# Performance work log

Measured on AMD Instinct MI355X. Metric: run time of the kernel, lower is better.

The kernel has to match this reference:

```python
import jax, jax.numpy as jnp
import numpy as np

MARGIN = 1.0  # init kwarg margin; top_k=None; reduction='mean'


def setup_inputs() -> dict:
    key = jax.random.key(0)
    k1, k2, k3 = jax.random.split(key, 3)
    B, H = 16384, 64
    scores = jax.random.normal(k1, (B, H), dtype=jnp.float32)
    rankings = jax.random.randint(k2, (B, H), 0, 65, dtype=jnp.int32)
    mask = jax.random.randint(k3, (B, H), 0, 2, dtype=jnp.int32).astype(jnp.bool_)
    return {"scores": scores, "rankings": rankings, "mask": mask}


def reference(scores, rankings, mask):
    # valid horses: present in race AND have a positive ranking
    valid = mask & (rankings > 0)                      # [B,H]
    # pair (i,j) counts iff both valid and rank_i < rank_j (implies i!=j)
    pair = (valid[:, :, None] & valid[:, None, :]
            & (rankings[:, :, None] < rankings[:, None, :]))  # [B,H,H]
    # hinge: clamp(margin - (s_i - s_j), min=0)
    hinge = jnp.maximum(MARGIN - (scores[:, :, None] - scores[:, None, :]), 0.0)
    pair_f = pair.astype(scores.dtype)
    num_pairs = pair_f.sum(axis=(1, 2))                # [B]
    batch_loss = (hinge * pair_f).sum(axis=(1, 2)) / jnp.maximum(num_pairs, 1.0)
    has = (num_pairs > 0).astype(scores.dtype)         # races contributing to mean
    n_valid = has.sum()
    total = (batch_loss * has).sum()
    # reduction='mean' over races with at least one pair; 0.0 if none
    return jnp.where(n_valid > 0, total / jnp.maximum(n_valid, 1.0),
                     jnp.asarray(0.0, scores.dtype))
```

## Files before the change

kernel.cpp:

```cpp
#include <hip/hip_runtime.h>

#define H 64
#define WPB 4
#define BLOCKS 1024

__global__ __launch_bounds__(WPB * 64)
void prl_races(const float* __restrict__ scores,
               const int* __restrict__ rankings,
               const int* __restrict__ mask,
               float2* __restrict__ partial, int B)
{
    __shared__ float4 smem[WPB][H / 2];
    __shared__ float wsum[WPB], wcnt[WPB];

    const int lane   = threadIdx.x & 63;
    const int wv     = threadIdx.x >> 6;
    const int gwave  = blockIdx.x * WPB + wv;
    const int nwaves = gridDim.x * WPB;
    const int iters  = (B + nwaves - 1) / nwaves;

    float loc_sum = 0.0f, loc_has = 0.0f;

    for (int it = 0; it < iters; ++it) {
        const int race  = gwave + it * nwaves;
        const bool act  = race < B;

        float s = 0.0f;
        int key = 0;
        if (act) {
            const int idx = race * H + lane;
            s = scores[idx];
            const int r = rankings[idx];
            const int m = mask[idx];
            key = (m != 0 && r > 0) ? r : 0;
        }

        float2* sm2 = reinterpret_cast<float2*>(&smem[wv][0]);
        sm2[lane] = make_float2(s, __int_as_float(key));
        __syncthreads();

        const float t = 1.0f - s;
        float sum = 0.0f, cnt = 0.0f;
        #pragma unroll
        for (int jj = 0; jj < H / 2; ++jj) {
            const float4 p = smem[wv][jj];
            const int k0 = __float_as_int(p.y);
            const int k1 = __float_as_int(p.w);
            const float h0 = fmaxf(t + p.x, 0.0f);
            const float h1 = fmaxf(t + p.z, 0.0f);
            if (key < k0) { sum += h0; cnt += 1.0f; }
            if (key < k1) { sum += h1; cnt += 1.0f; }
        }
        if (key == 0) { sum = 0.0f; cnt = 0.0f; }

        #pragma unroll
        for (int off = 32; off > 0; off >>= 1) {
            sum += __shfl_down(sum, off, 64);
            cnt += __shfl_down(cnt, off, 64);
        }
        if (lane == 0 && cnt > 0.0f) {
            loc_sum += sum / cnt;
            loc_has += 1.0f;
        }
        __syncthreads();
    }

    if (lane == 0) { wsum[wv] = loc_sum; wcnt[wv] = loc_has; }
    __syncthreads();
    if (threadIdx.x == 0) {
        float s = 0.0f, c = 0.0f;
        #pragma unroll
        for (int w = 0; w < WPB; ++w) { s += wsum[w]; c += wcnt[w]; }
        partial[blockIdx.x] = make_float2(s, c);
    }
}

__global__ __launch_bounds__(256)
void prl_reduce(const float2* __restrict__ partial, float* __restrict__ out, int n)
{
    __shared__ float ss[4], sc[4];
    const int lane = threadIdx.x & 63;
    const int wv   = threadIdx.x >> 6;

    float s = 0.0f, c = 0.0f;
    for (int i = threadIdx.x; i < n; i += 256) {
        const float2 p = partial[i];
        s += p.x; c += p.y;
    }
    #pragma unroll
    for (int off = 32; off > 0; off >>= 1) {
        s += __shfl_down(s, off, 64);
        c += __shfl_down(c, off, 64);
    }
    if (lane == 0) { ss[wv] = s; sc[wv] = c; }
    __syncthreads();
    if (threadIdx.x == 0) {
        float ts = ss[0] + ss[1] + ss[2] + ss[3];
        float tc = sc[0] + sc[1] + sc[2] + sc[3];
        out[0] = (tc > 0.0f) ? ts / tc : 0.0f;
    }
}

extern "C" void kernel_launch(void* const* d_in, const int* in_sizes, int n_in,
                              void* d_out, int out_size, void* d_ws, size_t ws_size,
                              hipStream_t stream)
{
    const float* scores   = (const float*)d_in[0];
    const int*   rankings = (const int*)d_in[1];
    const int*   mask     = (const int*)d_in[2];
    const int B = in_sizes[0] / H;

    float2* partial = (float2*)d_ws;

    prl_races<<<BLOCKS, WPB * 64, 0, stream>>>(scores, rankings, mask, partial, B);
    prl_reduce<<<1, 256, 0, stream>>>(partial, (float*)d_out, BLOCKS);
}
```

Before: 76.56 us.

## Use packed fp16 pairwise math with fdot2 and process two races per wave

Switches the pairwise hinge and rank-comparison computation to packed half-precision. Rank comparisons become clamped differences and are folded into an fdot2 accumulation. Each wave now loads two races up front into per-race shared buffers, the in-loop __syncthreads are dropped, and the grid grows to 2048 blocks. Converting scores and ranks to fp16 loses precision in the hinge and can break rank comparisons, since the clamped difference only works as a step function for integer ranks. The per-race count is accumulated in fp16 and the final partial reduce now reads more partials.

```diff
diff --git a/kernel.cpp b/kernel.cpp
--- a/kernel.cpp
+++ b/kernel.cpp
@@ -2,7 +2,12 @@
 
 #define H 64
 #define WPB 4
-#define BLOCKS 1024
+#define RPW 2
+
+typedef _Float16 h2 __attribute__((ext_vector_type(2)));
+typedef _Float16 __attribute__((may_alias)) f16a;
+
+union U32H2 { unsigned int u; h2 h; };
 
 __global__ __launch_bounds__(WPB * 64)
 void prl_races(const float* __restrict__ scores,
@@ -10,48 +15,68 @@
                const int* __restrict__ mask,
                float2* __restrict__ partial, int B)
 {
-    __shared__ float4 smem[WPB][H / 2];
+    __shared__ uint4 smem[WPB][RPW][H / 4];
     __shared__ float wsum[WPB], wcnt[WPB];
 
     const int lane   = threadIdx.x & 63;
     const int wv     = threadIdx.x >> 6;
     const int gwave  = blockIdx.x * WPB + wv;
     const int nwaves = gridDim.x * WPB;
-    const int iters  = (B + nwaves - 1) / nwaves;
+
+    float s[RPW]; int key[RPW];
+    #pragma unroll
+    for (int it = 0; it < RPW; ++it) {
+        const int race = gwave + it * nwaves;
+        s[it] = 0.0f; key[it] = 0;
+        if (race < B) {
+            const int idx = race * H + lane;
+            s[it] = scores[idx];
+            const int r = rankings[idx];
+            const int m = mask[idx];
+            key[it] = (m != 0 && r > 0) ? r : 0;
+        }
+        char* wbase = (char*)&smem[wv][it][0];
+        const int g = lane >> 2, sl = (lane & 3) * 2;
+        *(f16a*)(wbase + g * 16 + sl)     = (_Float16)s[it];
+        *(f16a*)(wbase + g * 16 + 8 + sl) = (_Float16)(float)key[it];
+    }
 
     float loc_sum = 0.0f, loc_has = 0.0f;
 
-    for (int it = 0; it < iters; ++it) {
-        const int race  = gwave + it * nwaves;
-        const bool act  = race < B;
+    #pragma unroll
+    for (int it = 0; it < RPW; ++it) {
+        const h2 t2   = (h2)(_Float16)(1.0f - s[it]);
+        const h2 ki2  = (h2)(_Float16)(float)key[it];
+        const h2 zero = (h2)(_Float16)0.0f;
+        const h2 one  = (h2)(_Float16)1.0f;
 
-        float s = 0.0f;
-        int key = 0;
-        if (act) {
-            const int idx = race * H + lane;
-            s = scores[idx];
-            const int r = rankings[idx];
-            const int m = mask[idx];
-            key = (m != 0 && r > 0) ? r : 0;
+        float sumA = 0.0f, sumB = 0.0f;
+        h2 cntA = zero, cntB = zero;
+
+        #pragma unroll
+        for (int g = 0; g < H / 4; ++g) {
+            const uint4 q = smem[wv][it][g];
+            U32H2 ux, uy, uz, uw;
+            ux.u = q.x; uy.u = q.y; uz.u = q.z; uw.u = q.w;
+            const h2 hA = __builtin_elementwise_max(t2 + ux.h, zero);
+            const h2 hB = __builtin_elementwise_max(t2 + uy.h, zero);
+            const h2 pA = __builtin_elementwise_min(__builtin_elementwise_max(uz.h - ki2, zero), one);
+            const h2 pB = __builtin_elementwise_min(__builtin_elementwise_max(uw.h - ki2, zero), one);
+#if __has_builtin(__builtin_amdgcn_fdot2)
+            sumA = __builtin_amdgcn_fdot2(hA, pA, sumA, false);
+            sumB = __builtin_amdgcn_fdot2(hB, pB, sumB, false);
+#else
+            sumA += (float)hA.x * (float)pA.x + (float)hA.y * (float)pA.y;
+            sumB += (float)hB.x * (float)pB.x + (float)hB.y * (float)pB.y;
+#endif
+            cntA = cntA + pA;
+            cntB = cntB + pB;
         }
 
-        float2* sm2 = reinterpret_cast<float2*>(&smem[wv][0]);
-        sm2[lane] = make_float2(s, __int_as_float(key));
-        __syncthreads();
-
-        const float t = 1.0f - s;
-        float sum = 0.0f, cnt = 0.0f;
-        #pragma unroll
-        for (int jj = 0; jj < H / 2; ++jj) {
-            const float4 p = smem[wv][jj];
-            const int k0 = __float_as_int(p.y);
-            const int k1 = __float_as_int(p.w);
-            const float h0 = fmaxf(t + p.x, 0.0f);
-            const float h1 = fmaxf(t + p.z, 0.0f);
-            if (key < k0) { sum += h0; cnt += 1.0f; }
-            if (key < k1) { sum += h1; cnt += 1.0f; }
-        }
-        if (key == 0) { sum = 0.0f; cnt = 0.0f; }
+        float sum = sumA + sumB;
+        const h2 c2 = cntA + cntB;
+        float cnt = (float)c2.x + (float)c2.y;
+        if (key[it] == 0) { sum = 0.0f; cnt = 0.0f; }
 
         #pragma unroll
         for (int off = 32; off > 0; off >>= 1) {
@@ -62,16 +87,15 @@
             loc_sum += sum / cnt;
             loc_has += 1.0f;
         }
-        __syncthreads();
     }
 
     if (lane == 0) { wsum[wv] = loc_sum; wcnt[wv] = loc_has; }
     __syncthreads();
     if (threadIdx.x == 0) {
-        float s = 0.0f, c = 0.0f;
+        float ps = 0.0f, pc = 0.0f;
         #pragma unroll
-        for (int w = 0; w < WPB; ++w) { s += wsum[w]; c += wcnt[w]; }
-        partial[blockIdx.x] = make_float2(s, c);
+        for (int w = 0; w < WPB; ++w) { ps += wsum[w]; pc += wcnt[w]; }
+        partial[blockIdx.x] = make_float2(ps, pc);
     }
 }
 
@@ -95,8 +119,8 @@
     if (lane == 0) { ss[wv] = s; sc[wv] = c; }
     __syncthreads();
     if (threadIdx.x == 0) {
-        float ts = ss[0] + ss[1] + ss[2] + ss[3];
-        float tc = sc[0] + sc[1] + sc[2] + sc[3];
+        const float ts = ss[0] + ss[1] + ss[2] + ss[3];
+        const float tc = sc[0] + sc[1] + sc[2] + sc[3];
         out[0] = (tc > 0.0f) ? ts / tc : 0.0f;
     }
 }
@@ -112,6 +136,7 @@
 
     float2* partial = (float2*)d_ws;
 
-    prl_races<<<BLOCKS, WPB * 64, 0, stream>>>(scores, rankings, mask, partial, B);
-    prl_reduce<<<1, 256, 0, stream>>>(partial, (float*)d_out, BLOCKS);
+    const int grid = (B + WPB * RPW - 1) / (WPB * RPW);
+    prl_races<<<grid, WPB * 64, 0, stream>>>(scores, rankings, mask, partial, B);
+    prl_reduce<<<1, 256, 0, stream>>>(partial, (float*)d_out, grid);
 }
```

New measurement: 74.43 us. -2.8%, faster.
